# Kernel optimization log

Hardware: AMD Instinct MI355X
Metric: run time of the kernel (lower is better)

## Reference

```python
import jax, jax.numpy as jnp
import numpy as np

N = 512            # input_size == number of graph nodes (X = I_N)
B = 64             # batch_size
H1, H2, H3 = 128, 64, 32   # hidden3 + 16 must equal 32 + class_nums
OUT = 8            # output_size; OUT*OUT + OUT == 72 (controller out channels)
CLS = 16           # class_nums (one-hot task encoding is 16-dim)


def setup_inputs():
    key = jax.random.key(0)
    ks = jax.random.split(key, 20)

    def u(k, shape, fan_out):
        s = 1.0 / np.sqrt(fan_out)
        return jax.random.uniform(k, shape, jnp.float32, -s, s)

    inp = {
        "adj": jax.random.uniform(ks[0], (B, 2, N, N), jnp.float32),
        "task_id": jax.random.randint(ks[1], (B,), 0, CLS),
    }
    dims = [(N, H1), (H1, H2), (H2, H3), (H3, OUT)]
    i = 2
    for pref in ("p", "n"):
        for l, (fi, fo) in enumerate(dims, 1):
            inp[f"w{l}{pref}"] = u(ks[i], (fi, fo), fo); i += 1
            inp[f"b{l}{pref}"] = u(ks[i], (fo,), fo); i += 1
    # controller: Conv1d(H3+CLS, 72, kernel=1, bias=False) -> stored as [72, H3+CLS]
    inp["wc"] = jax.random.normal(ks[i], (OUT * OUT + OUT, H3 + CLS), jnp.float32) * np.sqrt(2.0 / (OUT * OUT + OUT))
    return inp


def _normalize(adj):
    # D^-1/2 (A + I) D^-1/2, fully vectorized over [B, 2] (original loops in Python)
    a = adj + jnp.eye(adj.shape[-1], dtype=adj.dtype)
    d = a.sum(-1) ** -0.5                       # [B,2,N]
    return d[..., :, None] * a * d[..., None, :]


def _leaky(x):
    return jnp.where(x >= 0, x, 0.2 * x)


def _gcn_branch(feat, ws, bs):
    # feat: [B,N,N] normalized adjacency; X = I_N so first support = W1
    x = jnp.eye(N, dtype=feat.dtype)
    for i, (w, b) in enumerate(zip(ws, bs)):
        x = jnp.matmul(feat, jnp.matmul(x, w)) + b   # [B,N,fo]
        if i < len(ws) - 1:
            x = _leaky(x)
        if i == len(ws) - 2:
            conv3 = x
    return conv3, x                                  # ([B,N,H3], [B,N,OUT])


def _dcl(conv3, task_enc, conv4, wc):
    # conv3: [B,N,H3]; conv4: [B,N,OUT]; task_enc: [B,CLS]
    x_feat = conv3.mean(axis=1)                       # AdaptiveAvgPool1d over nodes -> [B,H3]
    x_cond = jnp.concatenate([x_feat, task_enc], 1)   # [B,H3+CLS]
    params = x_cond @ wc.T                            # [B,72]
    w = params[:, :OUT * OUT].reshape(B, OUT, OUT)    # per-sample dynamic head weights
    b = params[:, OUT * OUT:]                         # [B,OUT]
    # head_inputs = conv4.view(1,-1,N) with groups=B grouped conv1d (kernel 1)
    head = conv4.reshape(B, OUT, N)
    logits = jnp.einsum('boi,bin->bon', w, head) + b[..., None]   # [B,OUT,N]
    return logits.reshape(B, N, OUT)                  # faithful to torch reshape(N_,H_,-1)


def _forward(adj, task_id, w1p, b1p, w2p, b2p, w3p, b3p, w4p, b4p,
             w1n, b1n, w2n, b2n, w3n, b3n, w4n, b4n, wc):
    adj_n = _normalize(adj)
    feat_p, feat_n = adj_n[:, 0], adj_n[:, 1]
    p3, p4 = _gcn_branch(feat_p, [w1p, w2p, w3p, w4p], [b1p, b2p, b3p, b4p])
    n3, n4 = _gcn_branch(feat_n, [w1n, w2n, w3n, w4n], [b1n, b2n, b3n, b4n])
    te = jax.nn.one_hot(task_id, CLS, dtype=adj.dtype)   # encoding_task
    lp = _dcl(p3, te, p4, wc)
    ln = _dcl(n3, te, n4, wc)
    cc = jnp.concatenate([lp, ln], -1).reshape(-1, 2, N, OUT)  # [B,2,N,OUT]
    # F.dropout treated as identity (eval-mode determinism for reference)
    xm = jnp.matmul(cc, jnp.swapaxes(cc, -1, -2))              # [B,2,N,N]
    return jax.nn.log_sigmoid(xm) * -1.0


def reference(adj, task_id, w1p, b1p, w2p, b2p, w3p, b3p, w4p, b4p,
              w1n, b1n, w2n, b2n, w3n, b3n, w4n, b4n, wc):
    return _forward(adj, task_id, w1p, b1p, w2p, b2p, w3p, b3p, w4p, b4p,
                    w1n, b1n, w2n, b2n, w3n, b3n, w4n, b4n, wc)
```

## Files before the change

kernel.cpp:

```cpp
#include <hip/hip_runtime.h>
#include <math.h>

#define NN 512
#define NBC 128

typedef __attribute__((ext_vector_type(8))) __bf16 v8bf;
typedef __attribute__((ext_vector_type(4))) float v4f;

__device__ __forceinline__ void bsplit(float v, unsigned short& h, unsigned short& l) {
    unsigned u  = __builtin_bit_cast(unsigned, v);
    unsigned hb = (u + 0x7fffu + ((u >> 16) & 1u)) & 0xffff0000u;
    float hf    = __builtin_bit_cast(float, hb);
    h = (unsigned short)(hb >> 16);
    float lof   = v - hf;
    unsigned ul = __builtin_bit_cast(unsigned, lof);
    l = (unsigned short)((ul + 0x7fffu + ((ul >> 16) & 1u)) >> 16);
}

__global__ __launch_bounds__(256) void k_rowsum(const float* __restrict__ adj,
                                                float* __restrict__ dinv) {
    int wave = blockIdx.x * 4 + (threadIdx.x >> 6);
    int lane = threadIdx.x & 63;
    const float4* row = (const float4*)(adj + (size_t)wave * NN);
    float4 v0 = row[lane], v1 = row[lane + 64];
    float s = v0.x + v0.y + v0.z + v0.w + v1.x + v1.y + v1.z + v1.w;
    #pragma unroll
    for (int off = 32; off; off >>= 1) s += __shfl_down(s, off, 64);
    if (lane == 0) dinv[wave] = rsqrtf(1.0f + s);
}

__global__ __launch_bounds__(256) void k_convert(const float* __restrict__ adj,
    const float* __restrict__ dinv, unsigned short* __restrict__ anh,
    unsigned short* __restrict__ anl)
{
    unsigned gid = blockIdx.x * 256 + threadIdx.x;
    unsigned e = gid * 4;
    unsigned bc = e >> 18, rem = e & 0x3ffffu;
    unsigned i = rem >> 9, j = rem & 511u;
    float4 a = *(const float4*)(adj + (size_t)e);
    float di = dinv[bc * NN + i];
    const float4 dj = *(const float4*)(dinv + bc * NN + j);
    float v0 = di * dj.x * (a.x + ((j + 0) == i ? 1.f : 0.f));
    float v1 = di * dj.y * (a.y + ((j + 1) == i ? 1.f : 0.f));
    float v2 = di * dj.z * (a.z + ((j + 2) == i ? 1.f : 0.f));
    float v3 = di * dj.w * (a.w + ((j + 3) == i ? 1.f : 0.f));
    ushort4 hh, ll;
    bsplit(v0, hh.x, ll.x); bsplit(v1, hh.y, ll.y);
    bsplit(v2, hh.z, ll.z); bsplit(v3, hh.w, ll.w);
    *(ushort4*)(anh + e) = hh;
    *(ushort4*)(anl + e) = ll;
}

struct WJob  { const float* w; unsigned short* dh; unsigned short* dl; int HI; int HO; int HOP; };
struct WJobs { WJob j[8]; };
__global__ __launch_bounds__(256) void k_wprep(WJobs jobs) {
    WJob jb = jobs.j[blockIdx.y];
    int idx = blockIdx.x * 256 + threadIdx.x;
    if (idx >= jb.HOP * jb.HI) return;
    int h = idx / jb.HI, p = idx % jb.HI;
    float v = (h < jb.HO) ? jb.w[p * jb.HO + h] : 0.f;
    unsigned short hh, ll; bsplit(v, hh, ll);
    jb.dh[idx] = hh; jb.dl[idx] = ll;
}

template<int BN, int OUTW, bool SHAREDZ, bool ACT, bool WBF>
__global__ __launch_bounds__(256, 2) void k_mfma(
    const unsigned short* __restrict__ anh_, const unsigned short* __restrict__ anl_,
    const unsigned short* __restrict__ zh_,  const unsigned short* __restrict__ zl_,
    const float* __restrict__ bp, const float* __restrict__ bn,
    float* __restrict__ xf, unsigned short* __restrict__ xh, unsigned short* __restrict__ xl)
{
    constexpr int C = BN / 16;
    const int bc = blockIdx.y, rb = blockIdx.x;
    const int t = threadIdx.x, w = t >> 6, lane = t & 63;
    const int m0 = lane & 15, quad = lane >> 4;
    const int rowbase = rb * 128 + w * 32;
    const int s = SHAREDZ ? (bc & 1) : bc;
    const unsigned short* pa_h = anh_ + ((size_t)bc * NN + rowbase + m0) * NN + quad * 8;
    const unsigned short* pa_l = anl_ + ((size_t)bc * NN + rowbase + m0) * NN + quad * 8;
    const unsigned short* pz_h = zh_ + ((size_t)s * BN + m0) * NN + quad * 8;
    const unsigned short* pz_l = zl_ + ((size_t)s * BN + m0) * NN + quad * 8;
    v4f acc[2][C];
    #pragma unroll
    for (int r = 0; r < 2; ++r)
        #pragma unroll
        for (int c = 0; c < C; ++c) acc[r][c] = (v4f){0.f, 0.f, 0.f, 0.f};

    for (int kb = 0; kb < 16; ++kb) {
        const int ko = kb * 32;
        v8bf zfh[C], zfl[C];
        #pragma unroll
        for (int c = 0; c < C; ++c) {
            zfh[c] = *(const v8bf*)(pz_h + (size_t)(c * 16) * NN + ko);
            zfl[c] = *(const v8bf*)(pz_l + (size_t)(c * 16) * NN + ko);
        }
        #pragma unroll
        for (int r = 0; r < 2; ++r) {
            v8bf ah = *(const v8bf*)(pa_h + (size_t)(r * 16) * NN + ko);
            v8bf al = *(const v8bf*)(pa_l + (size_t)(r * 16) * NN + ko);
            #pragma unroll
            for (int c = 0; c < C; ++c) {
                acc[r][c] = __builtin_amdgcn_mfma_f32_16x16x32_bf16(ah, zfh[c], acc[r][c], 0, 0, 0);
                acc[r][c] = __builtin_amdgcn_mfma_f32_16x16x32_bf16(ah, zfl[c], acc[r][c], 0, 0, 0);
                acc[r][c] = __builtin_amdgcn_mfma_f32_16x16x32_bf16(al, zfh[c], acc[r][c], 0, 0, 0);
            }
        }
    }
    const float* bias = (bc & 1) ? bn : bp;
    #pragma unroll
    for (int r = 0; r < 2; ++r)
        #pragma unroll
        for (int c = 0; c < C; ++c) {
            int col = c * 16 + m0;
            if (OUTW < BN && col >= OUTW) continue;
            float bv = bias[col];
            #pragma unroll
            for (int reg = 0; reg < 4; ++reg) {
                int row = rowbase + r * 16 + quad * 4 + reg;
                float v = acc[r][c][reg] + bv;
                if (ACT) v = v >= 0.f ? v : 0.2f * v;
                size_t oi = ((size_t)bc * NN + row) * OUTW + col;
                if (xf) xf[oi] = v;
                if (WBF) {
                    unsigned short hh, ll; bsplit(v, hh, ll);
                    xh[oi] = hh; xl[oi] = ll;
                }
            }
        }
}

template<int HI, int HOP>
__global__ __launch_bounds__(256) void k_zgemm(
    const unsigned short* __restrict__ wth, const unsigned short* __restrict__ wtl,
    const unsigned short* __restrict__ xh_, const unsigned short* __restrict__ xl_,
    unsigned short* __restrict__ zh_, unsigned short* __restrict__ zl_)
{
    constexpr int MT = HOP / 16, JW = 4 / MT, NT = 8 / JW;
    const int bc = blockIdx.y, jb = blockIdx.x;
    const int t = threadIdx.x, w = t >> 6, lane = t & 63;
    const int m0 = lane & 15, quad = lane >> 4;
    const int mt = w % MT, jseg = w / MT;
    const int n0 = jb * 128 + jseg * (128 / JW);
    const int s = bc & 1;
    const unsigned short* pw_h = wth + ((size_t)s * HOP + mt * 16 + m0) * HI + quad * 8;
    const unsigned short* pw_l = wtl + ((size_t)s * HOP + mt * 16 + m0) * HI + quad * 8;
    const unsigned short* px_h = xh_ + ((size_t)bc * NN + n0 + m0) * HI + quad * 8;
    const unsigned short* px_l = xl_ + ((size_t)bc * NN + n0 + m0) * HI + quad * 8;
    v4f acc[NT];
    #pragma unroll
    for (int c = 0; c < NT; ++c) acc[c] = (v4f){0.f, 0.f, 0.f, 0.f};
    #pragma unroll
    for (int ks = 0; ks < HI / 32; ++ks) {
        const int ko = ks * 32;
        v8bf awh = *(const v8bf*)(pw_h + ko);
        v8bf awl = *(const v8bf*)(pw_l + ko);
        #pragma unroll
        for (int c = 0; c < NT; ++c) {
            v8bf bxh = *(const v8bf*)(px_h + (size_t)(c * 16) * HI + ko);
            v8bf bxl = *(const v8bf*)(px_l + (size_t)(c * 16) * HI + ko);
            acc[c] = __builtin_amdgcn_mfma_f32_16x16x32_bf16(awh, bxh, acc[c], 0, 0, 0);
            acc[c] = __builtin_amdgcn_mfma_f32_16x16x32_bf16(awh, bxl, acc[c], 0, 0, 0);
            acc[c] = __builtin_amdgcn_mfma_f32_16x16x32_bf16(awl, bxh, acc[c], 0, 0, 0);
        }
    }
    #pragma unroll
    for (int c = 0; c < NT; ++c) {
        int j = n0 + c * 16 + m0;
        #pragma unroll
        for (int reg = 0; reg < 4; ++reg) {
            int h = mt * 16 + quad * 4 + reg;
            unsigned short hh, ll; bsplit(acc[c][reg], hh, ll);
            size_t oi = ((size_t)bc * HOP + h) * NN + j;
            zh_[oi] = hh; zl_[oi] = ll;
        }
    }
}

template<int H, int HP, bool SHARED, bool ACT>
__global__ __launch_bounds__(256) void k_biggemm(
    const float* __restrict__ adj, const float* __restrict__ zcg,
    const float* __restrict__ wp, const float* __restrict__ wn,
    const float* __restrict__ bp, const float* __restrict__ bn,
    const float* __restrict__ dinv, float* __restrict__ xout)
{
    constexpr int CPT = HP / 16;
    constexpr int KT = 64;
    __shared__ float a_s[64 * 68];
    __shared__ float z_s[KT * H];
    const int bc = blockIdx.y;
    const int rt = blockIdx.x;
    const int t  = threadIdx.x;
    const int tx = t & 15, ty = t >> 4;
    const float* A    = adj + (size_t)bc * NN * NN + (size_t)rt * 64 * NN;
    const float* dloc = dinv + bc * NN;
    const float* ZG   = SHARED ? ((bc & 1) ? wn : wp) : (zcg + (size_t)bc * NN * H);
    const float* bias = (bc & 1) ? bn : bp;
    float acc[4][CPT];
    #pragma unroll
    for (int r = 0; r < 4; ++r)
        #pragma unroll
        for (int u = 0; u < CPT; ++u) acc[r][u] = 0.f;
    for (int kb = 0; kb < NN; kb += KT) {
        __syncthreads();
        #pragma unroll
        for (int l = 0; l < 4; ++l) {
            int idx = t + l * 256;
            int r = idx >> 4, q = idx & 15;
            float4 v = *(const float4*)(A + (size_t)r * NN + kb + q * 4);
            *(float4*)(a_s + r * 68 + q * 4) = v;
        }
        constexpr int NZ4 = KT * H / 4;
        for (int idx = t; idx < NZ4; idx += 256) {
            int k = idx / (H / 4), hq = idx % (H / 4);
            float4 v = *(const float4*)(ZG + (size_t)(kb + k) * H + hq * 4);
            if (SHARED) {
                float dk = dloc[kb + k];
                v.x *= dk; v.y *= dk; v.z *= dk; v.w *= dk;
            }
            *(float4*)(z_s + k * H + hq * 4) = v;
        }
        __syncthreads();
        #pragma unroll 8
        for (int k = 0; k < KT; ++k) {
            float ar[4];
            #pragma unroll
            for (int r = 0; r < 4; ++r) ar[r] = a_s[(ty * 4 + r) * 68 + k];
            float zv[CPT];
            #pragma unroll
            for (int u = 0; u < CPT; ++u) {
                int h = tx * CPT + u;
                if (H < HP && h >= H) h = 0;
                zv[u] = z_s[k * H + h];
            }
            #pragma unroll
            for (int r = 0; r < 4; ++r)
                #pragma unroll
                for (int u = 0; u < CPT; ++u)
                    acc[r][u] += ar[r] * zv[u];
        }
    }
    #pragma unroll
    for (int r = 0; r < 4; ++r) {
        int i = rt * 64 + ty * 4 + r;
        float di = dloc[i];
        #pragma unroll
        for (int u = 0; u < CPT; ++u) {
            int h = tx * CPT + u;
            if (H < HP && h >= H) continue;
            float self = SHARED ? di * ZG[(size_t)i * H + h] : ZG[(size_t)i * H + h];
            float v = di * (acc[r][u] + self) + bias[h];
            if (ACT) v = v >= 0.f ? v : 0.2f * v;
            xout[((size_t)bc * NN + i) * H + h] = v;
        }
    }
}

template<int HI, int HO>
__global__ __launch_bounds__(256) void k_smallgemm(
    const float* __restrict__ xin, const float* __restrict__ wp,
    const float* __restrict__ wn, const float* __restrict__ dinv,
    float* __restrict__ zc)
{
    constexpr int CPT = (HO >= 16) ? HO / 16 : 1;
    constexpr int XS = HI + 4;
    __shared__ float x_s[32 * XS];
    __shared__ float w_s[HI * HO];
    const int bc = blockIdx.y, jt = blockIdx.x, t = threadIdx.x;
    const int tx = t & 15, ty = t >> 4;
    const float* W = (bc & 1) ? wn : wp;
    const float* X = xin + ((size_t)bc * NN + jt * 32) * HI;
    for (int idx = t; idx < HI * HO / 4; idx += 256)
        *(float4*)(w_s + idx * 4) = *(const float4*)(W + idx * 4);
    for (int idx = t; idx < 32 * HI / 4; idx += 256) {
        int r = idx / (HI / 4), q = idx % (HI / 4);
        *(float4*)(x_s + r * XS + q * 4) = *(const float4*)(X + (size_t)r * HI + q * 4);
    }
    __syncthreads();
    float acc[2][CPT];
    #pragma unroll
    for (int r = 0; r < 2; ++r)
        #pragma unroll
        for (int u = 0; u < CPT; ++u) acc[r][u] = 0.f;
    #pragma unroll 4
    for (int p = 0; p < HI; ++p) {
        float xr[2];
        #pragma unroll
        for (int r = 0; r < 2; ++r) xr[r] = x_s[(ty * 2 + r) * XS + p];
        float wv[CPT];
        #pragma unroll
        for (int u = 0; u < CPT; ++u) {
            int h = tx * CPT + u;
            if (HO < 16 && h >= HO) h = 0;
            wv[u] = w_s[p * HO + h];
        }
        #pragma unroll
        for (int r = 0; r < 2; ++r)
            #pragma unroll
            for (int u = 0; u < CPT; ++u) acc[r][u] += xr[r] * wv[u];
    }
    const float* dloc = dinv + bc * NN;
    #pragma unroll
    for (int r = 0; r < 2; ++r) {
        int j = jt * 32 + ty * 2 + r;
        float dj = dloc[j];
        #pragma unroll
        for (int u = 0; u < CPT; ++u) {
            int h = tx * CPT + u;
            if (HO < 16 && h >= HO) continue;
            zc[((size_t)bc * NN + j) * HO + h] = dj * acc[r][u];
        }
    }
}

__global__ __launch_bounds__(256) void k_dcl(
    const float* __restrict__ x3, const float* __restrict__ x4,
    const float* __restrict__ wc, const int* __restrict__ task,
    float* __restrict__ L)
{
    __shared__ float ps[8][32];
    __shared__ float xf[32];
    __shared__ float pr[72];
    const int bc = blockIdx.x, t = threadIdx.x;
    const float* X3 = x3 + (size_t)bc * NN * 32;
    {
        int col = t & 31, rg = t >> 5;
        float s = 0.f;
        for (int r = rg; r < NN; r += 8) s += X3[r * 32 + col];
        ps[rg][col] = s;
    }
    __syncthreads();
    if (t < 32) {
        float s = 0.f;
        #pragma unroll
        for (int g = 0; g < 8; ++g) s += ps[g][t];
        xf[t] = s * (1.0f / 512.0f);
    }
    __syncthreads();
    if (t < 72) {
        int tid = task[bc >> 1];
        const float* wr = wc + t * 48;
        float s = wr[32 + tid];
        #pragma unroll
        for (int j = 0; j < 32; ++j) s += wr[j] * xf[j];
        pr[t] = s;
    }
    __syncthreads();
    const float* X4 = x4 + (size_t)bc * 4096;
    float* Lb = L + (size_t)bc * 4096;
    #pragma unroll
    for (int rep = 0; rep < 2; ++rep) {
        int n = rep * 256 + t;
        float hi[8];
        #pragma unroll
        for (int i = 0; i < 8; ++i) hi[i] = X4[i * 512 + n];
        #pragma unroll
        for (int o = 0; o < 8; ++o) {
            float s = pr[64 + o];
            #pragma unroll
            for (int i = 0; i < 8; ++i) s += pr[o * 8 + i] * hi[i];
            Lb[o * 512 + n] = s;
        }
    }
}

#define SCP 520
__global__ __launch_bounds__(256) void k_final(const float* __restrict__ L,
                                               float* __restrict__ out)
{
    __shared__ float scT[8 * SCP];
    const int bcid = blockIdx.y;
    const int b = bcid >> 1, c = bcid & 1;
    const int nt = blockIdx.x, t = threadIdx.x;
    const float* Lp = L + (size_t)(b * 2) * 4096;
    const float* Ln = Lp + 4096;
    for (int rep = 0; rep < 16; ++rep) {
        int e = rep * 256 + t;
        int f = c * 4096 + e;
        int n = f >> 4, k = f & 15;
        float v = (k < 8) ? Lp[n * 8 + k] : Ln[n * 8 + k - 8];
        scT[(e & 7) * SCP + (e >> 3)] = v;
    }
    __syncthreads();
    const int tx = t & 63, ty = t >> 6;
    const int n0 = nt * 32 + ty * 8;
    float cn[8][8];
    #pragma unroll
    for (int o = 0; o < 8; ++o)
        #pragma unroll
        for (int i = 0; i < 8; ++i) cn[i][o] = scT[o * SCP + n0 + i];
    float* ob = out + (size_t)bcid * NN * NN;
    #pragma unroll 2
    for (int mg = 0; mg < 8; ++mg) {
        int m = tx + mg * 64;
        float cm[8];
        #pragma unroll
        for (int o = 0; o < 8; ++o) cm[o] = scT[o * SCP + m];
        #pragma unroll
        for (int i = 0; i < 8; ++i) {
            float s = 0.f;
            #pragma unroll
            for (int o = 0; o < 8; ++o) s += cn[i][o] * cm[o];
            float r = fmaxf(-s, 0.f) + __logf(1.0f + __expf(-fabsf(s)));
            ob[(size_t)(n0 + i) * NN + m] = r;
        }
    }
}

extern "C" void kernel_launch(void* const* d_in, const int* in_sizes, int n_in,
                              void* d_out, int out_size, void* d_ws, size_t ws_size,
                              hipStream_t stream)
{
    const float* adj = (const float*)d_in[0];
    const int*  task = (const int*)d_in[1];
    const float* w1p = (const float*)d_in[2];  const float* b1p = (const float*)d_in[3];
    const float* w2p = (const float*)d_in[4];  const float* b2p = (const float*)d_in[5];
    const float* w3p = (const float*)d_in[6];  const float* b3p = (const float*)d_in[7];
    const float* w4p = (const float*)d_in[8];  const float* b4p = (const float*)d_in[9];
    const float* w1n = (const float*)d_in[10]; const float* b1n = (const float*)d_in[11];
    const float* w2n = (const float*)d_in[12]; const float* b2n = (const float*)d_in[13];
    const float* w3n = (const float*)d_in[14]; const float* b3n = (const float*)d_in[15];
    const float* w4n = (const float*)d_in[16]; const float* b4n = (const float*)d_in[17];
    const float* wc  = (const float*)d_in[18];
    (void)in_sizes; (void)n_in; (void)out_size;

    const size_t NEED = 198004736ull;
    if (ws_size >= NEED) {
        char* base = (char*)d_ws;
        float*          dinv = (float*)(base + 0);
        unsigned short* anh  = (unsigned short*)(base + 262144);
        unsigned short* anl  = (unsigned short*)(base + 67371008);
        unsigned short* zt1h = (unsigned short*)(base + 134479872);
        unsigned short* zt1l = (unsigned short*)(base + 134742016);
        unsigned short* wt2h = (unsigned short*)(base + 135004160);
        unsigned short* wt2l = (unsigned short*)(base + 135036928);
        unsigned short* wt3h = (unsigned short*)(base + 135069696);
        unsigned short* wt3l = (unsigned short*)(base + 135077888);
        unsigned short* wt4h = (unsigned short*)(base + 135086080);
        unsigned short* wt4l = (unsigned short*)(base + 135088128);
        unsigned short* x1h  = (unsigned short*)(base + 135090176);
        unsigned short* x1l  = (unsigned short*)(base + 151867392);
        unsigned short* zt2h = (unsigned short*)(base + 168644608);
        unsigned short* zt2l = (unsigned short*)(base + 177033216);
        float*          x3f  = (float*)(base + 185421824);
        float*          x4f  = (float*)(base + 193810432);
        float*          L    = (float*)(base + 195907584);
        unsigned short* x2h = x1h,  *x2l = x1l;
        unsigned short* x3h = x1h,  *x3l = x1l;
        unsigned short* zt3h = zt2h, *zt3l = zt2l;
        unsigned short* zt4h = zt2h, *zt4l = zt2l;

        k_rowsum<<<dim3(NBC * NN / 4), 256, 0, stream>>>(adj, dinv);
        k_convert<<<dim3(32768), 256, 0, stream>>>(adj, dinv, anh, anl);
        WJobs jobs;
        jobs.j[0] = {w1p, zt1h,          zt1l,          512, 128, 128};
        jobs.j[1] = {w1n, zt1h + 65536,  zt1l + 65536,  512, 128, 128};
        jobs.j[2] = {w2p, wt2h,          wt2l,          128,  64,  64};
        jobs.j[3] = {w2n, wt2h + 8192,   wt2l + 8192,   128,  64,  64};
        jobs.j[4] = {w3p, wt3h,          wt3l,           64,  32,  32};
        jobs.j[5] = {w3n, wt3h + 2048,   wt3l + 2048,    64,  32,  32};
        jobs.j[6] = {w4p, wt4h,          wt4l,           32,   8,  16};
        jobs.j[7] = {w4n, wt4h + 512,    wt4l + 512,     32,   8,  16};
        k_wprep<<<dim3(256, 8), 256, 0, stream>>>(jobs);

        k_mfma<128, 128, true,  true,  true ><<<dim3(4, NBC), 256, 0, stream>>>(
            anh, anl, zt1h, zt1l, b1p, b1n, nullptr, x1h, x1l);
        k_zgemm<128, 64><<<dim3(4, NBC), 256, 0, stream>>>(wt2h, wt2l, x1h, x1l, zt2h, zt2l);
        k_mfma<64, 64, false, true,  true ><<<dim3(4, NBC), 256, 0, stream>>>(
            anh, anl, zt2h, zt2l, b2p, b2n, nullptr, x2h, x2l);
        k_zgemm<64, 32><<<dim3(4, NBC), 256, 0, stream>>>(wt3h, wt3l, x2h, x2l, zt3h, zt3l);
        k_mfma<32, 32, false, true,  true ><<<dim3(4, NBC), 256, 0, stream>>>(
            anh, anl, zt3h, zt3l, b3p, b3n, x3f, x3h, x3l);
        k_zgemm<32, 16><<<dim3(4, NBC), 256, 0, stream>>>(wt4h, wt4l, x3h, x3l, zt4h, zt4l);
        k_mfma<16, 8, false, false, false><<<dim3(4, NBC), 256, 0, stream>>>(
            anh, anl, zt4h, zt4l, b4p, b4n, x4f, nullptr, nullptr);
        k_dcl<<<dim3(NBC), 256, 0, stream>>>(x3f, x4f, wc, task, L);
        k_final<<<dim3(16, NBC), 256, 0, stream>>>(L, (float*)d_out);
    } else {
        float* ws   = (float*)d_ws;
        float* dinv = ws;
        float* XA   = ws + 65536;
        float* X3   = XA + 8388608;
        float* X4   = X3 + 2097152;
        float* L    = X4 + 524288;
        float* ZC   = L  + 524288;
        k_rowsum<<<dim3(NBC * NN / 4), 256, 0, stream>>>(adj, dinv);
        k_biggemm<128,128,true ,true ><<<dim3(8,128), 256, 0, stream>>>(adj, nullptr, w1p, w1n, b1p, b1n, dinv, XA);
        k_smallgemm<128,64><<<dim3(16,128), 256, 0, stream>>>(XA, w2p, w2n, dinv, ZC);
        k_biggemm<64,64,false,true ><<<dim3(8,128), 256, 0, stream>>>(adj, ZC, nullptr, nullptr, b2p, b2n, dinv, XA);
        k_smallgemm<64,32><<<dim3(16,128), 256, 0, stream>>>(XA, w3p, w3n, dinv, ZC);
        k_biggemm<32,32,false,true ><<<dim3(8,128), 256, 0, stream>>>(adj, ZC, nullptr, nullptr, b3p, b3n, dinv, X3);
        k_smallgemm<32,8><<<dim3(16,128), 256, 0, stream>>>(X3, w4p, w4n, dinv, ZC);
        k_biggemm<8,16,false,false><<<dim3(8,128), 256, 0, stream>>>(adj, ZC, nullptr, nullptr, b4p, b4n, dinv, X4);
        k_dcl<<<dim3(128), 256, 0, stream>>>(X3, X4, wc, task, L);
        k_final<<<dim3(16,128), 256, 0, stream>>>(L, (float*)d_out);
    }
}
```

Baseline: 567.1 us.

## Fuse normalization and all GCN layers into one persistent per-graph kernel

Replaces the rowsum, convert and seven per-layer MFMA/zgemm launches with a single kernel that runs one 1024-thread block per (batch, channel) graph. The block computes degree normalization and builds the bf16 hi/lo adjacency inside layer 1, then runs every layer in sequence. Operands move into a fragment-ordered layout staged through LDS with global_load_lds. This removes launch overhead and the separate normalization pass, but only 128 blocks run, which may underfill the GPU.

```diff
diff --git a/kernel.cpp b/kernel.cpp
--- a/kernel.cpp
+++ b/kernel.cpp
@@ -17,6 +17,22 @@
     l = (unsigned short)((ul + 0x7fffu + ((ul >> 16) & 1u)) >> 16);
 }
 
+__device__ __forceinline__ void gl_lds16(const unsigned short* g, unsigned short* l) {
+    __builtin_amdgcn_global_load_lds(
+        (const __attribute__((address_space(1))) void*)g,
+        (__attribute__((address_space(3))) void*)l, 16, 0, 0);
+}
+
+__device__ __forceinline__ size_t fragaddr(int n, int k, int kext) {
+    return ((size_t)(n >> 4) * (kext >> 5) + (k >> 5)) * 512
+         + (size_t)(((n & 15) + 16 * ((k >> 3) & 3)) * 8 + (k & 7));
+}
+template<int KEXT>
+__device__ __forceinline__ size_t fa(int n, int k) {
+    return ((size_t)(n >> 4) * (KEXT >> 5) + (k >> 5)) * 512
+         + (size_t)(((n & 15) + 16 * ((k >> 3) & 3)) * 8 + (k & 7));
+}
+
 __global__ __launch_bounds__(256) void k_rowsum(const float* __restrict__ adj,
                                                 float* __restrict__ dinv) {
     int wave = blockIdx.x * 4 + (threadIdx.x >> 6);
@@ -27,28 +43,6 @@
     #pragma unroll
     for (int off = 32; off; off >>= 1) s += __shfl_down(s, off, 64);
     if (lane == 0) dinv[wave] = rsqrtf(1.0f + s);
-}
-
-__global__ __launch_bounds__(256) void k_convert(const float* __restrict__ adj,
-    const float* __restrict__ dinv, unsigned short* __restrict__ anh,
-    unsigned short* __restrict__ anl)
-{
-    unsigned gid = blockIdx.x * 256 + threadIdx.x;
-    unsigned e = gid * 4;
-    unsigned bc = e >> 18, rem = e & 0x3ffffu;
-    unsigned i = rem >> 9, j = rem & 511u;
-    float4 a = *(const float4*)(adj + (size_t)e);
-    float di = dinv[bc * NN + i];
-    const float4 dj = *(const float4*)(dinv + bc * NN + j);
-    float v0 = di * dj.x * (a.x + ((j + 0) == i ? 1.f : 0.f));
-    float v1 = di * dj.y * (a.y + ((j + 1) == i ? 1.f : 0.f));
-    float v2 = di * dj.z * (a.z + ((j + 2) == i ? 1.f : 0.f));
-    float v3 = di * dj.w * (a.w + ((j + 3) == i ? 1.f : 0.f));
-    ushort4 hh, ll;
-    bsplit(v0, hh.x, ll.x); bsplit(v1, hh.y, ll.y);
-    bsplit(v2, hh.z, ll.z); bsplit(v3, hh.w, ll.w);
-    *(ushort4*)(anh + e) = hh;
-    *(ushort4*)(anl + e) = ll;
 }
 
 struct WJob  { const float* w; unsigned short* dh; unsigned short* dl; int HI; int HO; int HOP; };
@@ -60,26 +54,27 @@
     int h = idx / jb.HI, p = idx % jb.HI;
     float v = (h < jb.HO) ? jb.w[p * jb.HO + h] : 0.f;
     unsigned short hh, ll; bsplit(v, hh, ll);
-    jb.dh[idx] = hh; jb.dl[idx] = ll;
-}
-
-template<int BN, int OUTW, bool SHAREDZ, bool ACT, bool WBF>
-__global__ __launch_bounds__(256, 2) void k_mfma(
-    const unsigned short* __restrict__ anh_, const unsigned short* __restrict__ anl_,
-    const unsigned short* __restrict__ zh_,  const unsigned short* __restrict__ zl_,
-    const float* __restrict__ bp, const float* __restrict__ bn,
-    float* __restrict__ xf, unsigned short* __restrict__ xh, unsigned short* __restrict__ xl)
+    size_t oa = fragaddr(h, p, jb.HI);
+    jb.dh[oa] = hh; jb.dl[oa] = ll;
+}
+
+
+template<int BN, int OUTW, bool L1, bool ACT, bool WBF, bool XF>
+__device__ __forceinline__ void gcn_layer(
+    int bc, const float* __restrict__ adj, const float* __restrict__ dls,
+    const unsigned short* __restrict__ ansh, const unsigned short* __restrict__ ansl,
+    unsigned short* __restrict__ andh, unsigned short* __restrict__ andl,
+    const unsigned short* __restrict__ zgh, const unsigned short* __restrict__ zgl,
+    const float* __restrict__ bias,
+    unsigned short* __restrict__ xoh, unsigned short* __restrict__ xol,
+    float* __restrict__ xf,
+    unsigned short* aP0, unsigned short* aP1,
+    unsigned short* zP0, unsigned short* zP1)
 {
     constexpr int C = BN / 16;
-    const int bc = blockIdx.y, rb = blockIdx.x;
     const int t = threadIdx.x, w = t >> 6, lane = t & 63;
     const int m0 = lane & 15, quad = lane >> 4;
-    const int rowbase = rb * 128 + w * 32;
-    const int s = SHAREDZ ? (bc & 1) : bc;
-    const unsigned short* pa_h = anh_ + ((size_t)bc * NN + rowbase + m0) * NN + quad * 8;
-    const unsigned short* pa_l = anl_ + ((size_t)bc * NN + rowbase + m0) * NN + quad * 8;
-    const unsigned short* pz_h = zh_ + ((size_t)s * BN + m0) * NN + quad * 8;
-    const unsigned short* pz_l = zl_ + ((size_t)s * BN + m0) * NN + quad * 8;
+
     v4f acc[2][C];
     #pragma unroll
     for (int r = 0; r < 2; ++r)
@@ -87,93 +82,214 @@
         for (int c = 0; c < C; ++c) acc[r][c] = (v4f){0.f, 0.f, 0.f, 0.f};
 
     for (int kb = 0; kb < 16; ++kb) {
-        const int ko = kb * 32;
-        v8bf zfh[C], zfl[C];
+        __syncthreads();
+        if constexpr (L1) {
+            const int ci = t >> 2, cj = (t & 3) * 8;
+            #pragma unroll
+            for (int pass = 0; pass < 2; ++pass) {
+                const int i = pass * 256 + ci;
+                const int gj = kb * 32 + cj;
+                const float* ap = adj + (size_t)bc * NN * NN + (size_t)i * NN + gj;
+                float4 a0 = *(const float4*)ap;
+                float4 a1 = *(const float4*)(ap + 4);
+                const float di = dls[i];
+                const float4 d0 = *(const float4*)(dls + gj);
+                const float4 d1 = *(const float4*)(dls + gj + 4);
+                float av[8] = { a0.x,a0.y,a0.z,a0.w,a1.x,a1.y,a1.z,a1.w };
+                float dv[8] = { d0.x,d0.y,d0.z,d0.w,d1.x,d1.y,d1.z,d1.w };
+                unsigned pw[4], qw[4];
+                #pragma unroll
+                for (int q = 0; q < 4; ++q) {
+                    unsigned short h0, l0, h1, l1;
+                    float u0 = di * dv[2*q]   * (av[2*q]   + ((gj+2*q)   == i ? 1.f : 0.f));
+                    float u1 = di * dv[2*q+1] * (av[2*q+1] + ((gj+2*q+1) == i ? 1.f : 0.f));
+                    bsplit(u0, h0, l0); bsplit(u1, h1, l1);
+                    pw[q] = (unsigned)h0 | ((unsigned)h1 << 16);
+                    qw[q] = (unsigned)l0 | ((unsigned)l1 << 16);
+                }
+                const int lofs = (i >> 4) * 512 + ((i & 15) + 16 * (cj >> 3)) * 8;
+                const size_t go = ((size_t)(i >> 4) * 16 + kb) * 512
+                                + (size_t)(((i & 15) + 16 * (cj >> 3)) * 8);
+                uint4 ph; ph.x = pw[0]; ph.y = pw[1]; ph.z = pw[2]; ph.w = pw[3];
+                uint4 pl; pl.x = qw[0]; pl.y = qw[1]; pl.z = qw[2]; pl.w = qw[3];
+                *(uint4*)(aP0 + lofs) = ph;
+                *(uint4*)(aP1 + lofs) = pl;
+                *(uint4*)(andh + go) = ph;
+                *(uint4*)(andl + go) = pl;
+            }
+        } else {
+            #pragma unroll
+            for (int q = 0; q < 2; ++q) {
+                const int c0 = q * 1024 + (t & ~63);
+                const int c  = c0 + lane;
+                const size_t go = ((size_t)(c >> 6) * 16 + kb) * 512 + (size_t)((c & 63) * 8);
+                gl_lds16(ansh + go, aP0 + (size_t)c0 * 8);
+                gl_lds16(ansl + go, aP1 + (size_t)c0 * 8);
+            }
+        }
+        if (t < BN * 4) {
+            const int c0 = t & ~63, c = t;
+            const size_t go = ((size_t)(c >> 6) * 16 + kb) * 512 + (size_t)((c & 63) * 8);
+            gl_lds16(zgh + go, zP0 + (size_t)c0 * 8);
+            gl_lds16(zgl + go, zP1 + (size_t)c0 * 8);
+        }
+        __syncthreads();
+
+        const int r0 = w * 2;
+        v8bf ah0 = *(const v8bf*)(aP0 + (size_t)(r0    ) * 512 + lane * 8);
+        v8bf al0 = *(const v8bf*)(aP1 + (size_t)(r0    ) * 512 + lane * 8);
+        v8bf ah1 = *(const v8bf*)(aP0 + (size_t)(r0 + 1) * 512 + lane * 8);
+        v8bf al1 = *(const v8bf*)(aP1 + (size_t)(r0 + 1) * 512 + lane * 8);
         #pragma unroll
         for (int c = 0; c < C; ++c) {
-            zfh[c] = *(const v8bf*)(pz_h + (size_t)(c * 16) * NN + ko);
-            zfl[c] = *(const v8bf*)(pz_l + (size_t)(c * 16) * NN + ko);
-        }
+            v8bf zfh = *(const v8bf*)(zP0 + (size_t)c * 512 + lane * 8);
+            v8bf zfl = *(const v8bf*)(zP1 + (size_t)c * 512 + lane * 8);
+            acc[0][c] = __builtin_amdgcn_mfma_f32_16x16x32_bf16(ah0, zfh, acc[0][c], 0, 0, 0);
+            acc[0][c] = __builtin_amdgcn_mfma_f32_16x16x32_bf16(ah0, zfl, acc[0][c], 0, 0, 0);
+            acc[0][c] = __builtin_amdgcn_mfma_f32_16x16x32_bf16(al0, zfh, acc[0][c], 0, 0, 0);
+            acc[1][c] = __builtin_amdgcn_mfma_f32_16x16x32_bf16(ah1, zfh, acc[1][c], 0, 0, 0);
+            acc[1][c] = __builtin_amdgcn_mfma_f32_16x16x32_bf16(ah1, zfl, acc[1][c], 0, 0, 0);
+            acc[1][c] = __builtin_amdgcn_mfma_f32_16x16x32_bf16(al1, zfh, acc[1][c], 0, 0, 0);
+        }
+    }
+
+    #pragma unroll
+    for (int c = 0; c < C; ++c) {
+        int col = c * 16 + m0;
+        if (OUTW < BN && col >= OUTW) continue;
+        float bv = bias[col];
         #pragma unroll
         for (int r = 0; r < 2; ++r) {
-            v8bf ah = *(const v8bf*)(pa_h + (size_t)(r * 16) * NN + ko);
-            v8bf al = *(const v8bf*)(pa_l + (size_t)(r * 16) * NN + ko);
-            #pragma unroll
-            for (int c = 0; c < C; ++c) {
-                acc[r][c] = __builtin_amdgcn_mfma_f32_16x16x32_bf16(ah, zfh[c], acc[r][c], 0, 0, 0);
-                acc[r][c] = __builtin_amdgcn_mfma_f32_16x16x32_bf16(ah, zfl[c], acc[r][c], 0, 0, 0);
-                acc[r][c] = __builtin_amdgcn_mfma_f32_16x16x32_bf16(al, zfh[c], acc[r][c], 0, 0, 0);
-            }
-        }
-    }
-    const float* bias = (bc & 1) ? bn : bp;
-    #pragma unroll
-    for (int r = 0; r < 2; ++r)
-        #pragma unroll
-        for (int c = 0; c < C; ++c) {
-            int col = c * 16 + m0;
-            if (OUTW < BN && col >= OUTW) continue;
-            float bv = bias[col];
             #pragma unroll
             for (int reg = 0; reg < 4; ++reg) {
-                int row = rowbase + r * 16 + quad * 4 + reg;
+                int row = w * 32 + r * 16 + quad * 4 + reg;
                 float v = acc[r][c][reg] + bv;
                 if (ACT) v = v >= 0.f ? v : 0.2f * v;
-                size_t oi = ((size_t)bc * NN + row) * OUTW + col;
-                if (xf) xf[oi] = v;
-                if (WBF) {
+                if constexpr (XF) xf[(size_t)row * OUTW + col] = v;
+                if constexpr (WBF) {
                     unsigned short hh, ll; bsplit(v, hh, ll);
-                    xh[oi] = hh; xl[oi] = ll;
+                    size_t o = fa<BN>(row, col);
+                    xoh[o] = hh; xol[o] = ll;
                 }
             }
         }
-}
-
-template<int HI, int HOP>
-__global__ __launch_bounds__(256) void k_zgemm(
+    }
+}
+
+template<int HOP, int HI>
+__device__ __forceinline__ void gcn_zgemm(
     const unsigned short* __restrict__ wth, const unsigned short* __restrict__ wtl,
-    const unsigned short* __restrict__ xh_, const unsigned short* __restrict__ xl_,
-    unsigned short* __restrict__ zh_, unsigned short* __restrict__ zl_)
-{
-    constexpr int MT = HOP / 16, JW = 4 / MT, NT = 8 / JW;
-    const int bc = blockIdx.y, jb = blockIdx.x;
+    const unsigned short* __restrict__ xgh, const unsigned short* __restrict__ xgl,
+    unsigned short* __restrict__ zoh, unsigned short* __restrict__ zol,
+    unsigned short* aP0, unsigned short* aP1)
+{
+    constexpr int HT = HOP / 16, JG = 16 / HT, JT = 32 / JG, KS = HI / 32;
     const int t = threadIdx.x, w = t >> 6, lane = t & 63;
     const int m0 = lane & 15, quad = lane >> 4;
-    const int mt = w % MT, jseg = w / MT;
-    const int n0 = jb * 128 + jseg * (128 / JW);
-    const int s = bc & 1;
-    const unsigned short* pw_h = wth + ((size_t)s * HOP + mt * 16 + m0) * HI + quad * 8;
-    const unsigned short* pw_l = wtl + ((size_t)s * HOP + mt * 16 + m0) * HI + quad * 8;
-    const unsigned short* px_h = xh_ + ((size_t)bc * NN + n0 + m0) * HI + quad * 8;
-    const unsigned short* px_l = xl_ + ((size_t)bc * NN + n0 + m0) * HI + quad * 8;
-    v4f acc[NT];
-    #pragma unroll
-    for (int c = 0; c < NT; ++c) acc[c] = (v4f){0.f, 0.f, 0.f, 0.f};
-    #pragma unroll
-    for (int ks = 0; ks < HI / 32; ++ks) {
-        const int ko = ks * 32;
-        v8bf awh = *(const v8bf*)(pw_h + ko);
-        v8bf awl = *(const v8bf*)(pw_l + ko);
-        #pragma unroll
-        for (int c = 0; c < NT; ++c) {
-            v8bf bxh = *(const v8bf*)(px_h + (size_t)(c * 16) * HI + ko);
-            v8bf bxl = *(const v8bf*)(px_l + (size_t)(c * 16) * HI + ko);
-            acc[c] = __builtin_amdgcn_mfma_f32_16x16x32_bf16(awh, bxh, acc[c], 0, 0, 0);
-            acc[c] = __builtin_amdgcn_mfma_f32_16x16x32_bf16(awh, bxl, acc[c], 0, 0, 0);
-            acc[c] = __builtin_amdgcn_mfma_f32_16x16x32_bf16(awl, bxh, acc[c], 0, 0, 0);
-        }
-    }
-    #pragma unroll
-    for (int c = 0; c < NT; ++c) {
-        int j = n0 + c * 16 + m0;
+    const int hf = w % HT, jg = w / HT;
+    v4f acc[JT];
+    #pragma unroll
+    for (int c = 0; c < JT; ++c) acc[c] = (v4f){0.f, 0.f, 0.f, 0.f};
+
+    for (int ks = 0; ks < KS; ++ks) {
+        __syncthreads();
+        #pragma unroll
+        for (int q = 0; q < 2; ++q) {
+            const int c0 = q * 1024 + (t & ~63);
+            const int c  = c0 + lane;
+            const size_t go = ((size_t)(c >> 6) * KS + ks) * 512 + (size_t)((c & 63) * 8);
+            gl_lds16(xgh + go, aP0 + (size_t)c0 * 8);
+            gl_lds16(xgl + go, aP1 + (size_t)c0 * 8);
+        }
+        __syncthreads();
+        const size_t wo = ((size_t)hf * KS + ks) * 512 + (size_t)(lane * 8);
+        v8bf wh = *(const v8bf*)(wth + wo);
+        v8bf wl = *(const v8bf*)(wtl + wo);
+        #pragma unroll
+        for (int c = 0; c < JT; ++c) {
+            const int jt = jg * JT + c;
+            v8bf bxh = *(const v8bf*)(aP0 + (size_t)jt * 512 + lane * 8);
+            v8bf bxl = *(const v8bf*)(aP1 + (size_t)jt * 512 + lane * 8);
+            acc[c] = __builtin_amdgcn_mfma_f32_16x16x32_bf16(wh, bxh, acc[c], 0, 0, 0);
+            acc[c] = __builtin_amdgcn_mfma_f32_16x16x32_bf16(wh, bxl, acc[c], 0, 0, 0);
+            acc[c] = __builtin_amdgcn_mfma_f32_16x16x32_bf16(wl, bxh, acc[c], 0, 0, 0);
+        }
+    }
+    #pragma unroll
+    for (int c = 0; c < JT; ++c) {
+        int j = (jg * JT + c) * 16 + m0;
         #pragma unroll
         for (int reg = 0; reg < 4; ++reg) {
-            int h = mt * 16 + quad * 4 + reg;
+            int h = hf * 16 + quad * 4 + reg;
             unsigned short hh, ll; bsplit(acc[c][reg], hh, ll);
-            size_t oi = ((size_t)bc * HOP + h) * NN + j;
-            zh_[oi] = hh; zl_[oi] = ll;
-        }
-    }
+            size_t o = fa<512>(h, j);
+            zoh[o] = hh; zol[o] = ll;
+        }
+    }
+}
+
+__global__ __launch_bounds__(1024) void k_gcn(
+    const float* __restrict__ adj,
+    const unsigned short* __restrict__ zt1h, const unsigned short* __restrict__ zt1l,
+    const unsigned short* __restrict__ wt2h, const unsigned short* __restrict__ wt2l,
+    const unsigned short* __restrict__ wt3h, const unsigned short* __restrict__ wt3l,
+    const unsigned short* __restrict__ wt4h, const unsigned short* __restrict__ wt4l,
+    const float* __restrict__ b1p, const float* __restrict__ b1n,
+    const float* __restrict__ b2p, const float* __restrict__ b2n,
+    const float* __restrict__ b3p, const float* __restrict__ b3n,
+    const float* __restrict__ b4p, const float* __restrict__ b4n,
+    unsigned short* __restrict__ anh, unsigned short* __restrict__ anl,
+    unsigned short* __restrict__ xh, unsigned short* __restrict__ xl,
+    unsigned short* __restrict__ zh, unsigned short* __restrict__ zl,
+    float* __restrict__ x3f, float* __restrict__ x4f)
+{
+    __shared__ __align__(16) unsigned short aP0[16384];
+    __shared__ __align__(16) unsigned short aP1[16384];
+    __shared__ __align__(16) unsigned short zP0[4096];
+    __shared__ __align__(16) unsigned short zP1[4096];
+    __shared__ float dls[512];
+
+    const int bc = blockIdx.x, s = bc & 1;
+    const int t = threadIdx.x, w = t >> 6, lane = t & 63;
+
+    {
+        const float* A0 = adj + (size_t)bc * NN * NN;
+        for (int rr = 0; rr < 32; ++rr) {
+            int row = w * 32 + rr;
+            const float4* rp = (const float4*)(A0 + (size_t)row * NN);
+            float4 v0 = rp[lane], v1 = rp[lane + 64];
+            float sm = v0.x + v0.y + v0.z + v0.w + v1.x + v1.y + v1.z + v1.w;
+            #pragma unroll
+            for (int off = 32; off; off >>= 1) sm += __shfl_down(sm, off, 64);
+            if (lane == 0) dls[row] = sm;
+        }
+        __syncthreads();
+        if (t < 512) dls[t] = rsqrtf(1.0f + dls[t]);
+    }
+
+    unsigned short* anb_h = anh + (size_t)bc * 262144;
+    unsigned short* anb_l = anl + (size_t)bc * 262144;
+    unsigned short* xb_h  = xh + (size_t)bc * 65536;
+    unsigned short* xb_l  = xl + (size_t)bc * 65536;
+    unsigned short* zb_h  = zh + (size_t)bc * 32768;
+    unsigned short* zb_l  = zl + (size_t)bc * 32768;
+
+    gcn_layer<128, 128, true, true, true, false>(bc, adj, dls,
+        nullptr, nullptr, anb_h, anb_l,
+        zt1h + s * 65536, zt1l + s * 65536, s ? b1n : b1p,
+        xb_h, xb_l, nullptr, aP0, aP1, zP0, zP1);
+    gcn_zgemm<64, 128>(wt2h + s * 8192, wt2l + s * 8192, xb_h, xb_l, zb_h, zb_l, aP0, aP1);
+    gcn_layer<64, 64, false, true, true, false>(bc, adj, dls,
+        anb_h, anb_l, nullptr, nullptr,
+        zb_h, zb_l, s ? b2n : b2p, xb_h, xb_l, nullptr, aP0, aP1, zP0, zP1);
+    gcn_zgemm<32, 64>(wt3h + s * 2048, wt3l + s * 2048, xb_h, xb_l, zb_h, zb_l, aP0, aP1);
+    gcn_layer<32, 32, false, true, true, true>(bc, adj, dls,
+        anb_h, anb_l, nullptr, nullptr,
+        zb_h, zb_l, s ? b3n : b3p, xb_h, xb_l, x3f + (size_t)bc * 16384, aP0, aP1, zP0, zP1);
+    gcn_zgemm<16, 32>(wt4h + s * 512, wt4l + s * 512, xb_h, xb_l, zb_h, zb_l, aP0, aP1);
+    gcn_layer<16, 8, false, false, false, true>(bc, adj, dls,
+        anb_h, anb_l, nullptr, nullptr,
+        zb_h, zb_l, s ? b4n : b4p, nullptr, nullptr, x4f + (size_t)bc * 4096, aP0, aP1, zP0, zP1);
 }
 
 template<int H, int HP, bool SHARED, bool ACT>
@@ -423,34 +539,27 @@
     const float* wc  = (const float*)d_in[18];
     (void)in_sizes; (void)n_in; (void)out_size;
 
-    const size_t NEED = 198004736ull;
+    const size_t NEED = 197742592ull;
     if (ws_size >= NEED) {
         char* base = (char*)d_ws;
-        float*          dinv = (float*)(base + 0);
-        unsigned short* anh  = (unsigned short*)(base + 262144);
-        unsigned short* anl  = (unsigned short*)(base + 67371008);
-        unsigned short* zt1h = (unsigned short*)(base + 134479872);
-        unsigned short* zt1l = (unsigned short*)(base + 134742016);
-        unsigned short* wt2h = (unsigned short*)(base + 135004160);
-        unsigned short* wt2l = (unsigned short*)(base + 135036928);
-        unsigned short* wt3h = (unsigned short*)(base + 135069696);
-        unsigned short* wt3l = (unsigned short*)(base + 135077888);
-        unsigned short* wt4h = (unsigned short*)(base + 135086080);
-        unsigned short* wt4l = (unsigned short*)(base + 135088128);
-        unsigned short* x1h  = (unsigned short*)(base + 135090176);
-        unsigned short* x1l  = (unsigned short*)(base + 151867392);
-        unsigned short* zt2h = (unsigned short*)(base + 168644608);
-        unsigned short* zt2l = (unsigned short*)(base + 177033216);
-        float*          x3f  = (float*)(base + 185421824);
-        float*          x4f  = (float*)(base + 193810432);
-        float*          L    = (float*)(base + 195907584);
-        unsigned short* x2h = x1h,  *x2l = x1l;
-        unsigned short* x3h = x1h,  *x3l = x1l;
-        unsigned short* zt3h = zt2h, *zt3l = zt2l;
-        unsigned short* zt4h = zt2h, *zt4l = zt2l;
-
-        k_rowsum<<<dim3(NBC * NN / 4), 256, 0, stream>>>(adj, dinv);
-        k_convert<<<dim3(32768), 256, 0, stream>>>(adj, dinv, anh, anl);
+        unsigned short* anh  = (unsigned short*)(base + 0);
+        unsigned short* anl  = (unsigned short*)(base + 67108864);
+        unsigned short* xh   = (unsigned short*)(base + 134217728);
+        unsigned short* xl   = (unsigned short*)(base + 150994944);
+        unsigned short* zh   = (unsigned short*)(base + 167772160);
+        unsigned short* zl   = (unsigned short*)(base + 176160768);
+        unsigned short* zt1h = (unsigned short*)(base + 184549376);
+        unsigned short* zt1l = (unsigned short*)(base + 184811520);
+        unsigned short* wt2h = (unsigned short*)(base + 185073664);
+        unsigned short* wt2l = (unsigned short*)(base + 185106432);
+        unsigned short* wt3h = (unsigned short*)(base + 185139200);
+        unsigned short* wt3l = (unsigned short*)(base + 185147392);
+        unsigned short* wt4h = (unsigned short*)(base + 185155584);
+        unsigned short* wt4l = (unsigned short*)(base + 185157632);
+        float*          x3f  = (float*)(base + 185159680);
+        float*          x4f  = (float*)(base + 193548288);
+        float*          L    = (float*)(base + 195645440);
+
         WJobs jobs;
         jobs.j[0] = {w1p, zt1h,          zt1l,          512, 128, 128};
         jobs.j[1] = {w1n, zt1h + 65536,  zt1l + 65536,  512, 128, 128};
@@ -462,17 +571,11 @@
         jobs.j[7] = {w4n, wt4h + 512,    wt4l + 512,     32,   8,  16};
         k_wprep<<<dim3(256, 8), 256, 0, stream>>>(jobs);
 
-        k_mfma<128, 128, true,  true,  true ><<<dim3(4, NBC), 256, 0, stream>>>(
-            anh, anl, zt1h, zt1l, b1p, b1n, nullptr, x1h, x1l);
-        k_zgemm<128, 64><<<dim3(4, NBC), 256, 0, stream>>>(wt2h, wt2l, x1h, x1l, zt2h, zt2l);
-        k_mfma<64, 64, false, true,  true ><<<dim3(4, NBC), 256, 0, stream>>>(
-            anh, anl, zt2h, zt2l, b2p, b2n, nullptr, x2h, x2l);
-        k_zgemm<64, 32><<<dim3(4, NBC), 256, 0, stream>>>(wt3h, wt3l, x2h, x2l, zt3h, zt3l);
-        k_mfma<32, 32, false, true,  true ><<<dim3(4, NBC), 256, 0, stream>>>(
-            anh, anl, zt3h, zt3l, b3p, b3n, x3f, x3h, x3l);
-        k_zgemm<32, 16><<<dim3(4, NBC), 256, 0, stream>>>(wt4h, wt4l, x3h, x3l, zt4h, zt4l);
-        k_mfma<16, 8, false, false, false><<<dim3(4, NBC), 256, 0, stream>>>(
-            anh, anl, zt4h, zt4l, b4p, b4n, x4f, nullptr, nullptr);
+        k_gcn<<<dim3(NBC), 1024, 0, stream>>>(adj,
+            zt1h, zt1l, wt2h, wt2l, wt3h, wt3l, wt4h, wt4l,
+            b1p, b1n, b2p, b2n, b3p, b3n, b4p, b4n,
+            anh, anl, xh, xl, zh, zl, x3f, x4f);
+
         k_dcl<<<dim3(NBC), 256, 0, stream>>>(x3f, x4f, wc, task, L);
         k_final<<<dim3(16, NBC), 256, 0, stream>>>(L, (float*)d_out);
     } else {
```

New measurement: 551.4 us. 1.03x faster.
